# Kernel tuning notes

Measured on AMD Instinct MI355X. Metric: run time of the kernel, lower is better.

The kernel has to match this reference:

```python
import jax, jax.numpy as jnp
import numpy as np


def setup_inputs() -> dict:
    key = jax.random.key(0)
    k1, k2, k3, k4 = jax.random.split(key, 4)
    B, C, H, W = 8, 64, 64, 64
    Ck = C // 8  # query/key channels
    x = jax.random.normal(k1, (B, C, H, W), dtype=jnp.float32)
    # 1x1 conv1d weights (bias=False); spectral norm only rescales the weight,
    # so plain matrices are math-equivalent at a given parameter value.
    wq = jax.random.normal(k2, (Ck, C), dtype=jnp.float32) * (1.0 / np.sqrt(C))
    wk = jax.random.normal(k3, (Ck, C), dtype=jnp.float32) * (1.0 / np.sqrt(C))
    wv = jax.random.normal(k4, (C, C), dtype=jnp.float32) * (1.0 / np.sqrt(C))
    gamma = jnp.array([0.5], dtype=jnp.float32)  # nonzero so attention path is exercised
    return {"x": x, "wq": wq, "wk": wk, "wv": wv, "gamma": gamma}


def reference(x, wq, wk, wv, gamma):
    B, C, H, W = x.shape
    xf = x.reshape(B, C, H * W)                      # [B, C, N]
    f = jnp.einsum('kc,bcn->bkn', wq, xf)            # [B, C/8, N]
    g = jnp.einsum('kc,bcn->bkn', wk, xf)            # [B, C/8, N]
    h = jnp.einsum('oc,bcn->bon', wv, xf)            # [B, C,   N]
    scores = jnp.einsum('bkn,bkm->bnm', f, g)        # f^T g, [B, N, N]
    beta = jax.nn.softmax(scores, axis=1)            # softmax over dim=1 (rows), as in torch
    o = jnp.einsum('bcn,bnm->bcm', h, beta)          # [B, C, N]
    out = gamma[0] * o + xf
    return out.reshape(B, C, H, W)
```

## Files before the change

kernel.cpp:

```cpp
#include <hip/hip_runtime.h>
#include <hip/hip_bf16.h>

typedef __bf16 bf16x8 __attribute__((ext_vector_type(8)));
typedef float f32x4 __attribute__((ext_vector_type(4)));
typedef float f32x16 __attribute__((ext_vector_type(16)));
typedef unsigned int uint2v __attribute__((ext_vector_type(2)));

#define MFMA16 __builtin_amdgcn_mfma_f32_16x16x32_bf16
#define MFMA32 __builtin_amdgcn_mfma_f32_32x32x16_bf16

__device__ __forceinline__ unsigned short f2b(float f) {
  unsigned int u = __float_as_uint(f);
  u += 0x7FFFu + ((u >> 16) & 1u);
  return (unsigned short)(u >> 16);
}

__device__ __forceinline__ float b2f(unsigned short s) {
  return __uint_as_float(((unsigned)s) << 16);
}

union U128 {
  uint4 u;
  unsigned short s[8];
  bf16x8 b;
};

union BPack {
  __hip_bfloat162 h2;
  unsigned u;
};

__device__ __forceinline__ unsigned packbf(float a, float b) {
  BPack p;
  p.h2 = __float22bfloat162_rn(make_float2(a, b));
  return p.u;
}

__global__ __launch_bounds__(256, 2) void proj_kernel(
    const float* __restrict__ x, const float* __restrict__ wq,
    const float* __restrict__ wk, const float* __restrict__ wv_w,
    unsigned short* __restrict__ f_t, unsigned short* __restrict__ g_t,
    unsigned short* __restrict__ h_out) {
  __shared__ unsigned short xT[64 * 64];
  __shared__ unsigned short wT[96 * 72];

  const int tid = (int)threadIdx.x;
  const int wvp = tid >> 6;
  const int lane = tid & 63;
  const int b = (int)blockIdx.x & 7;
  const int n0 = ((int)blockIdx.x >> 3) << 6;

  {
    const float* xb = x + ((size_t)b << 18) + n0 + lane;
    const int c0 = wvp * 16;
    float xv[16];
#pragma unroll
    for (int cc = 0; cc < 16; ++cc) xv[cc] = xb[(size_t)(c0 + cc) << 12];
#pragma unroll
    for (int p = 0; p < 4; ++p) {
      const int c = c0 + 4 * p;
      uint2 d;
      d.x = packbf(xv[4 * p + 0], xv[4 * p + 1]);
      d.y = packbf(xv[4 * p + 2], xv[4 * p + 3]);
      const int g = c >> 3;
      const int idx = lane * 64 + (((g ^ (lane & 7)) << 3) | (((c >> 2) & 1) << 2));
      *(uint2*)&xT[idx] = d;
    }
  }
#pragma unroll
  for (int i = 0; i < 20; ++i) {
    const int idx = i * 256 + tid;
    const float wval = (idx < 512) ? wq[idx] * 1.44269504f
                     : (idx < 1024) ? wk[idx - 512]
                                    : wv_w[idx - 1024];
    wT[(idx >> 6) * 72 + (idx & 63)] = f2b(wval);
  }
  __syncthreads();

  const int t = lane & 15, q = lane >> 4;
  const int nloc = wvp * 16 + t;
  U128 Bf[2];
#pragma unroll
  for (int kp = 0; kp < 2; ++kp) {
    const int g = kp * 4 + q;
    Bf[kp].u = *(const uint4*)&xT[nloc * 64 + ((g ^ (nloc & 7)) << 3)];
  }
  const int nabs = n0 + nloc;
#pragma unroll
  for (int rt = 0; rt < 5; ++rt) {
    f32x4 acc = {0.f, 0.f, 0.f, 0.f};
#pragma unroll
    for (int kp = 0; kp < 2; ++kp) {
      U128 Af;
      Af.u = *(const uint4*)&wT[(rt * 16 + t) * 72 + ((kp * 4 + q) << 3)];
      acc = MFMA16(Af.b, Bf[kp].b, acc, 0, 0, 0);
    }
#pragma unroll
    for (int reg = 0; reg < 4; ++reg) {
      const int r = rt * 16 + 4 * q + reg;
      const unsigned short v = f2b(acc[reg]);
      if (r < 8)
        f_t[((size_t)((b << 12) + nabs) << 3) + r] = v;
      else if (r < 16)
        g_t[((size_t)((b << 12) + nabs) << 3) + (r - 8)] = v;
      else
        h_out[((size_t)b << 18) + ((size_t)(nabs >> 3) << 9) +
              ((r - 16) << 3) + (nabs & 7)] = v;
    }
  }
}

__global__ __launch_bounds__(256, 4) void attn_kernel(
    const unsigned short* __restrict__ f_t, const unsigned short* __restrict__ g_t,
    const unsigned short* __restrict__ h, const float* __restrict__ x,
    const float* __restrict__ gamma, float* __restrict__ out) {
  __shared__ unsigned short Opart[4][32][66];
  __shared__ float lred[4][32];
  __shared__ float lsum[32];

  const int tid = (int)threadIdx.x;
  const int wave = tid >> 6;
  const int lane = tid & 63;
  const int ml = lane & 31;
  const int hh = lane >> 5;

  const int b = (int)blockIdx.x & 7;
  const int m32 = ((int)blockIdx.x >> 3) << 5;

  const unsigned short* fb = f_t + ((size_t)b << 15);
  const unsigned short* hb = h + ((size_t)b << 18);

  U128 G;
  G.u = make_uint4(0u, 0u, 0u, 0u);
  if (hh == 0) G.u = *(const uint4*)(g_t + ((size_t)((b << 12) + m32 + ml) << 3));

  f32x16 O0 = {}, O1 = {};
  float lp = 0.f;
  const f32x16 ZC = {};

  const int nbase = wave << 10;

  const unsigned short* fp = fb + ((size_t)(nbase + ml) << 3);
  const unsigned short* hp = hb + ((nbase >> 3) << 9) + (hh << 9) + (ml << 3);

  U128 F0, F1, Ha_e[4], Ha_o[4];
  f32x16 S;

  F0.u = *(const uint4*)(fp);
  F1.u = *(const uint4*)(fp + 256);
  Ha_e[0].u = *(const uint4*)(hp);
  Ha_e[1].u = *(const uint4*)(hp + 256);
  Ha_e[2].u = *(const uint4*)(hp + 1024);
  Ha_e[3].u = *(const uint4*)(hp + 1280);
  __builtin_amdgcn_s_setprio(1);
  S = MFMA32(F0.b, G.b, ZC, 0, 0, 0);
  __builtin_amdgcn_s_setprio(0);

  auto body = [&](const U128* Hv, const U128& Fn, bool produce) {
    float e[16];
#pragma unroll
    for (int r = 0; r < 16; ++r) e[r] = __builtin_amdgcn_exp2f(S[r]);
    if (produce) {
      __builtin_amdgcn_s_setprio(1);
      S = MFMA32(Fn.b, G.b, ZC, 0, 0, 0);
      __builtin_amdgcn_s_setprio(0);
    }
    lp += (((e[0] + e[1]) + (e[2] + e[3])) + ((e[4] + e[5]) + (e[6] + e[7]))) +
          (((e[8] + e[9]) + (e[10] + e[11])) + ((e[12] + e[13]) + (e[14] + e[15])));
#pragma unroll
    for (int kt = 0; kt < 2; ++kt) {
      const unsigned A0 = packbf(e[8 * kt + 0], e[8 * kt + 1]);
      const unsigned A1 = packbf(e[8 * kt + 2], e[8 * kt + 3]);
      const unsigned B0 = packbf(e[8 * kt + 4], e[8 * kt + 5]);
      const unsigned B1 = packbf(e[8 * kt + 6], e[8 * kt + 7]);
      const uint2v r0 = __builtin_amdgcn_permlane32_swap(A0, B0, false, false);
      const uint2v r1 = __builtin_amdgcn_permlane32_swap(A1, B1, false, false);
      U128 P;
      P.u.x = r0[0];
      P.u.y = r1[0];
      P.u.z = r0[1];
      P.u.w = r1[1];
      __builtin_amdgcn_s_setprio(1);
      O0 = MFMA32(Hv[2 * kt + 0].b, P.b, O0, 0, 0, 0);
      O1 = MFMA32(Hv[2 * kt + 1].b, P.b, O1, 0, 0, 0);
      __builtin_amdgcn_s_setprio(0);
    }
  };

#pragma unroll 1
  for (int j = 0; j < 15; ++j) {
    Ha_o[0].u = *(const uint4*)(hp + 2048);
    Ha_o[1].u = *(const uint4*)(hp + 2304);
    Ha_o[2].u = *(const uint4*)(hp + 3072);
    Ha_o[3].u = *(const uint4*)(hp + 3328);
    F0.u = *(const uint4*)(fp + 512);
    body(Ha_e, F1, true);
    Ha_e[0].u = *(const uint4*)(hp + 4096);
    Ha_e[1].u = *(const uint4*)(hp + 4352);
    Ha_e[2].u = *(const uint4*)(hp + 5120);
    Ha_e[3].u = *(const uint4*)(hp + 5376);
    F1.u = *(const uint4*)(fp + 768);
    body(Ha_o, F0, true);
    fp += 512;
    hp += 4096;
  }
  Ha_o[0].u = *(const uint4*)(hp + 2048);
  Ha_o[1].u = *(const uint4*)(hp + 2304);
  Ha_o[2].u = *(const uint4*)(hp + 3072);
  Ha_o[3].u = *(const uint4*)(hp + 3328);
  body(Ha_e, F1, true);
  body(Ha_o, F1, false);

  lp += __shfl_xor(lp, 32, 64);
  if (hh == 0) lred[wave][ml] = lp;
#pragma unroll
  for (int r = 0; r < 8; ++r) {
    const int c0 = ((2 * r) & 3) + 8 * (r >> 1) + 4 * hh;
    *(unsigned*)&Opart[wave][ml][c0] = packbf(O0[2 * r], O0[2 * r + 1]);
    *(unsigned*)&Opart[wave][ml][c0 + 32] = packbf(O1[2 * r], O1[2 * r + 1]);
  }
  __syncthreads();
  if (tid < 32)
    lsum[tid] = (lred[0][tid] + lred[1][tid]) + (lred[2][tid] + lred[3][tid]);
  __syncthreads();

  const int c = tid >> 2;
  const int m0l = (tid & 3) << 3;
  const float gam = gamma[0];
  float a[8];
#pragma unroll
  for (int j = 0; j < 8; ++j) a[j] = 0.f;
#pragma unroll
  for (int w = 0; w < 4; ++w)
#pragma unroll
    for (int j = 0; j < 8; ++j) a[j] += b2f(Opart[w][m0l + j][c]);

  const f32x4 l0 = *(const f32x4*)&lsum[m0l];
  const f32x4 l1 = *(const f32x4*)&lsum[m0l + 4];
  const size_t oi = (((size_t)b * 64 + c) << 12) + m32 + m0l;
  f32x4 xo0 = *(const f32x4*)(x + oi);
  f32x4 xo1 = *(const f32x4*)(x + oi + 4);
#pragma unroll
  for (int j = 0; j < 4; ++j) {
    xo0[j] += gam / l0[j] * a[j];
    xo1[j] += gam / l1[j] * a[j + 4];
  }
  *(f32x4*)(out + oi) = xo0;
  *(f32x4*)(out + oi + 4) = xo1;
}

extern "C" void kernel_launch(void* const* d_in, const int* in_sizes, int n_in,
                              void* d_out, int out_size, void* d_ws, size_t ws_size,
                              hipStream_t stream) {
  (void)in_sizes; (void)n_in; (void)out_size; (void)ws_size;
  const float* x = (const float*)d_in[0];
  const float* wq = (const float*)d_in[1];
  const float* wk = (const float*)d_in[2];
  const float* wv = (const float*)d_in[3];
  const float* gamma = (const float*)d_in[4];
  float* out = (float*)d_out;

  unsigned short* f_t = (unsigned short*)d_ws;
  unsigned short* g_t = f_t + (size_t)8 * 4096 * 8;
  unsigned short* h = g_t + (size_t)8 * 4096 * 8;

  proj_kernel<<<512, 256, 0, stream>>>(x, wq, wk, wv, f_t, g_t, h);
  attn_kernel<<<1024, 256, 0, stream>>>(f_t, g_t, h, x, gamma, out);
}
```

Measured before the change: 105.5 us.

## Coalesce projection stores via LDS staging and halve attention epilogue LDS

The projection kernel now writes f/g as packed 8-byte stores and stages h through a shared-memory tile, so h is written to global memory in 16-byte coalesced chunks instead of scattered 2-byte stores. The attention kernel epilogue splits the cross-wave O reduction into two 16-row halves, halving the Opart shared buffer, which may raise occupancy. This costs an extra barrier in the projection kernel and two extra barriers in the attention epilogue.

Measured after the change: 102.9 us. 1.03x faster.

```diff
diff --git a/kernel.cpp b/kernel.cpp
--- a/kernel.cpp
+++ b/kernel.cpp
@@ -43,6 +43,7 @@
     unsigned short* __restrict__ h_out) {
   __shared__ unsigned short xT[64 * 64];
   __shared__ unsigned short wT[96 * 72];
+  __shared__ unsigned short hT[64 * 72];
 
   const int tid = (int)threadIdx.x;
   const int wvp = tid >> 6;
@@ -86,8 +87,23 @@
     Bf[kp].u = *(const uint4*)&xT[nloc * 64 + ((g ^ (nloc & 7)) << 3)];
   }
   const int nabs = n0 + nloc;
-#pragma unroll
-  for (int rt = 0; rt < 5; ++rt) {
+
+  {
+    f32x4 acc = {0.f, 0.f, 0.f, 0.f};
+#pragma unroll
+    for (int kp = 0; kp < 2; ++kp) {
+      U128 Af;
+      Af.u = *(const uint4*)&wT[t * 72 + ((kp * 4 + q) << 3)];
+      acc = MFMA16(Af.b, Bf[kp].b, acc, 0, 0, 0);
+    }
+    uint2 d;
+    d.x = packbf(acc[0], acc[1]);
+    d.y = packbf(acc[2], acc[3]);
+    unsigned short* dst = (q & 2) ? g_t : f_t;
+    *(uint2*)&dst[((size_t)((b << 12) + nabs) << 3) + ((q & 1) << 2)] = d;
+  }
+#pragma unroll
+  for (int rt = 1; rt < 5; ++rt) {
     f32x4 acc = {0.f, 0.f, 0.f, 0.f};
 #pragma unroll
     for (int kp = 0; kp < 2; ++kp) {
@@ -95,18 +111,22 @@
       Af.u = *(const uint4*)&wT[(rt * 16 + t) * 72 + ((kp * 4 + q) << 3)];
       acc = MFMA16(Af.b, Bf[kp].b, acc, 0, 0, 0);
     }
-#pragma unroll
-    for (int reg = 0; reg < 4; ++reg) {
-      const int r = rt * 16 + 4 * q + reg;
-      const unsigned short v = f2b(acc[reg]);
-      if (r < 8)
-        f_t[((size_t)((b << 12) + nabs) << 3) + r] = v;
-      else if (r < 16)
-        g_t[((size_t)((b << 12) + nabs) << 3) + (r - 8)] = v;
-      else
-        h_out[((size_t)b << 18) + ((size_t)(nabs >> 3) << 9) +
-              ((r - 16) << 3) + (nabs & 7)] = v;
-    }
+    const int cbase = (rt - 1) * 16 + 4 * q;
+#pragma unroll
+    for (int reg = 0; reg < 4; ++reg)
+      hT[(cbase + reg) * 72 + nloc] = f2b(acc[reg]);
+  }
+  __syncthreads();
+
+  {
+    const int hc = tid & 63;
+    const int hw = tid >> 6;
+    const uint4 v0 = *(const uint4*)&hT[hc * 72 + hw * 16];
+    const uint4 v1 = *(const uint4*)&hT[hc * 72 + hw * 16 + 8];
+    const size_t hbase =
+        ((size_t)b << 18) + ((size_t)((n0 + hw * 16) >> 3) << 9) + (hc << 3);
+    *(uint4*)&h_out[hbase] = v0;
+    *(uint4*)&h_out[hbase + 512] = v1;
   }
 }
 
@@ -114,7 +134,7 @@
     const unsigned short* __restrict__ f_t, const unsigned short* __restrict__ g_t,
     const unsigned short* __restrict__ h, const float* __restrict__ x,
     const float* __restrict__ gamma, float* __restrict__ out) {
-  __shared__ unsigned short Opart[4][32][66];
+  __shared__ unsigned short Opart[4][16][66];
   __shared__ float lred[4][32];
   __shared__ float lsum[32];
 
@@ -213,40 +233,51 @@
 
   lp += __shfl_xor(lp, 32, 64);
   if (hh == 0) lred[wave][ml] = lp;
-#pragma unroll
-  for (int r = 0; r < 8; ++r) {
-    const int c0 = ((2 * r) & 3) + 8 * (r >> 1) + 4 * hh;
-    *(unsigned*)&Opart[wave][ml][c0] = packbf(O0[2 * r], O0[2 * r + 1]);
-    *(unsigned*)&Opart[wave][ml][c0 + 32] = packbf(O1[2 * r], O1[2 * r + 1]);
-  }
+
+  const float gam = gamma[0];
+
+  auto stash = [&](int p) {
+    if ((ml >> 4) == p) {
+      const int mi = ml & 15;
+#pragma unroll
+      for (int r = 0; r < 8; ++r) {
+        const int c0 = ((2 * r) & 3) + 8 * (r >> 1) + 4 * hh;
+        *(unsigned*)&Opart[wave][mi][c0] = packbf(O0[2 * r], O0[2 * r + 1]);
+        *(unsigned*)&Opart[wave][mi][c0 + 32] = packbf(O1[2 * r], O1[2 * r + 1]);
+      }
+    }
+  };
+  auto drain = [&](int p) {
+    const int c = tid >> 2;
+    const int m4 = (tid & 3) << 2;
+    float a0 = 0.f, a1 = 0.f, a2 = 0.f, a3 = 0.f;
+#pragma unroll
+    for (int w = 0; w < 4; ++w) {
+      a0 += b2f(Opart[w][m4 + 0][c]);
+      a1 += b2f(Opart[w][m4 + 1][c]);
+      a2 += b2f(Opart[w][m4 + 2][c]);
+      a3 += b2f(Opart[w][m4 + 3][c]);
+    }
+    const f32x4 l = *(const f32x4*)&lsum[p * 16 + m4];
+    const size_t oi = (((size_t)b * 64 + c) << 12) + m32 + p * 16 + m4;
+    f32x4 xo = *(const f32x4*)(x + oi);
+    xo[0] += gam / l[0] * a0;
+    xo[1] += gam / l[1] * a1;
+    xo[2] += gam / l[2] * a2;
+    xo[3] += gam / l[3] * a3;
+    *(f32x4*)(out + oi) = xo;
+  };
+
+  stash(0);
   __syncthreads();
   if (tid < 32)
     lsum[tid] = (lred[0][tid] + lred[1][tid]) + (lred[2][tid] + lred[3][tid]);
   __syncthreads();
-
-  const int c = tid >> 2;
-  const int m0l = (tid & 3) << 3;
-  const float gam = gamma[0];
-  float a[8];
-#pragma unroll
-  for (int j = 0; j < 8; ++j) a[j] = 0.f;
-#pragma unroll
-  for (int w = 0; w < 4; ++w)
-#pragma unroll
-    for (int j = 0; j < 8; ++j) a[j] += b2f(Opart[w][m0l + j][c]);
-
-  const f32x4 l0 = *(const f32x4*)&lsum[m0l];
-  const f32x4 l1 = *(const f32x4*)&lsum[m0l + 4];
-  const size_t oi = (((size_t)b * 64 + c) << 12) + m32 + m0l;
-  f32x4 xo0 = *(const f32x4*)(x + oi);
-  f32x4 xo1 = *(const f32x4*)(x + oi + 4);
-#pragma unroll
-  for (int j = 0; j < 4; ++j) {
-    xo0[j] += gam / l0[j] * a[j];
-    xo1[j] += gam / l1[j] * a[j + 4];
-  }
-  *(f32x4*)(out + oi) = xo0;
-  *(f32x4*)(out + oi + 4) = xo1;
+  drain(0);
+  __syncthreads();
+  stash(1);
+  __syncthreads();
+  drain(1);
 }
 
 extern "C" void kernel_launch(void* const* d_in, const int* in_sizes, int n_in,
```
